# Performance work log

Measured on AMD Instinct MI355X. Metric: run time of the kernel, lower is better.

## Reference

```python
import jax, jax.numpy as jnp
import numpy as np

B, S, D, M = 4, 2048, 1024, 4  # batch, seq_len, d_model, n_stride_masks


def setup_inputs() -> dict:
    key = jax.random.key(0)
    ks = jax.random.split(key, 10)
    lin = lambda k: jax.random.normal(k, (D, D), jnp.float32) / np.float32(np.sqrt(D))
    return {
        "x": jax.random.normal(ks[0], (B, S, D), jnp.float32),
        "stride_masks": jax.random.randint(ks[1], (M, S, S), 0, 2, jnp.int32),
        "Wq": lin(ks[2]), "bq": jnp.zeros((D,), jnp.float32),
        "Wk": lin(ks[3]), "bk": jnp.zeros((D,), jnp.float32),
        "Wv": lin(ks[4]), "bv": jnp.zeros((D,), jnp.float32),
        "Wo": lin(ks[5]), "bo": jnp.zeros((D,), jnp.float32),
    }


def reference(x, stride_masks, Wq, bq, Wk, bk, Wv, bv, Wo, bo):
    scale = jnp.float32(np.sqrt(D))
    Q = x @ Wq + bq  # [B,S,D]
    K = x @ Wk + bk
    V = x @ Wv + bv
    # scores are identical for every mask; compute once (same math as the loop)
    scores = jnp.einsum("bqd,bkd->bqk", Q, K) / scale  # [B,S,S]
    masked = jnp.where(stride_masks[:, None] == 0, jnp.float32(-1e9), scores[None])  # [M,B,S,S]
    weights = jax.nn.softmax(masked, axis=-1)
    # sum over masks then divide by M == mean(stack(outs), 0)
    out = jnp.einsum("mbqk,bkd->bqd", weights, V) / jnp.float32(M)
    return out @ Wo + bo
```

## Files before the change

kernel.cpp:

```cpp
#include <hip/hip_runtime.h>
#include <hip/hip_bf16.h>
#include <stdint.h>

#define B_ 4
#define S_ 2048
#define D_ 1024
#define M_ 4

typedef __bf16 bf16;
typedef _Float16 f16;
typedef unsigned char u8;
typedef __bf16 bf16x8 __attribute__((ext_vector_type(8)));
typedef _Float16 f16x8 __attribute__((ext_vector_type(8)));
typedef float f32x4 __attribute__((ext_vector_type(4)));

__device__ __forceinline__ void async_copy16(const void* g, void* l) {
  __builtin_amdgcn_global_load_lds(
      (const __attribute__((address_space(1))) void*)g,
      (__attribute__((address_space(3))) void*)l, 16, 0, 0);
}

__global__ __launch_bounds__(256) void prep(
    const float* __restrict__ x, const float* __restrict__ w0,
    const float* __restrict__ w1, const float* __restrict__ w2,
    const float* __restrict__ w3, const int* __restrict__ masks,
    bf16* __restrict__ xc, bf16* __restrict__ WT, u8* __restrict__ pk) {
  __shared__ bf16 t[64][65];
  const int blk = blockIdx.x;
  const int tid = threadIdx.x;
  const long SS = (long)S_ * S_;

  if (blk < 4096) {
    const long i = (long)blk * 2048 + tid * 8;
    const float4 a = *(const float4*)(x + i);
    const float4 b = *(const float4*)(x + i + 4);
    bf16x8 o;
    o[0] = (bf16)a.x; o[1] = (bf16)a.y; o[2] = (bf16)a.z; o[3] = (bf16)a.w;
    o[4] = (bf16)b.x; o[5] = (bf16)b.y; o[6] = (bf16)b.z; o[7] = (bf16)b.w;
    *(bf16x8*)(xc + i) = o;
  } else if (blk < 5120) {
    const int local = blk - 4096;
    const int z = local >> 8;
    const int rem = local & 255;
    const int r0 = (rem >> 4) * 64;
    const int c0 = (rem & 15) * 64;
    const int tx = tid & 63;
    const int ty = tid >> 6;
    const float* in = (z == 0) ? w0 : (z == 1) ? w1 : (z == 2) ? w2 : w3;
    bf16* out = WT + (long)z * D_ * D_;
    for (int i = ty; i < 64; i += 4)
      t[i][tx] = (bf16)in[(long)(r0 + i) * D_ + c0 + tx];
    __syncthreads();
    for (int i = ty; i < 64; i += 4)
      out[(long)(c0 + i) * D_ + r0 + tx] = t[tx][i];
  } else {
    const long e = (long)(blk - 5120) * 2048 + tid * 8;
    unsigned long long wv = 0;
#pragma unroll
    for (int m = 0; m < M_; ++m) {
      const int4 a = *(const int4*)(masks + m * SS + e);
      const int4 b = *(const int4*)(masks + m * SS + e + 4);
      const int v[8] = {a.x, a.y, a.z, a.w, b.x, b.y, b.z, b.w};
#pragma unroll
      for (int j = 0; j < 8; ++j)
        wv |= (unsigned long long)(v[j] != 0 ? 1u : 0u) << (8 * j + m);
    }
    *(unsigned long long*)(pk + e) = wv;
  }
}

__global__ __launch_bounds__(256) void transposeB(
    const bf16* __restrict__ in, bf16* __restrict__ out,
    int rows, int cols, long ib, long ob) {
  __shared__ bf16 t[64][65];
  in += (long)blockIdx.z * ib;
  out += (long)blockIdx.z * ob;
  const int r0 = blockIdx.y * 64;
  const int c0 = blockIdx.x * 64;
  const int tx = threadIdx.x & 63;
  const int ty = threadIdx.x >> 6;
#pragma unroll
  for (int i = ty; i < 64; i += 4) t[i][tx] = in[(long)(r0 + i) * cols + c0 + tx];
  __syncthreads();
#pragma unroll
  for (int i = ty; i < 64; i += 4) out[(long)(c0 + i) * rows + r0 + tx] = t[tx][i];
}

#define MODE_PLAIN 0
#define MODE_EXP 1
#define MODE_QKV 2
#define MODE_PV 3

template <typename OutT, int MODE>
__global__ __launch_bounds__(512) void gemmA(
    const bf16* __restrict__ A, int lda,
    const bf16* __restrict__ Bt, long bzs, int ldb,
    OutT* __restrict__ C, int ldc,
    const float* __restrict__ bias0, const float* __restrict__ bias1,
    const float* __restrict__ bias2, float alpha, int K) {
  __shared__ __align__(16) bf16 As[3][256 * 32];
  __shared__ __align__(16) bf16 Bs[3][128 * 32];
  const int tid = threadIdx.x;
  const int lane = tid & 63;
  const int w = tid >> 6;
  const int wm = w & 3;
  const int wn = w >> 2;
  const int quad = lane >> 4;
  const int l15 = lane & 15;
  const int fse = (quad ^ ((l15 >> 1) & 3)) << 3;

  const int gx = gridDim.x;
  const int pid = blockIdx.y * gx + blockIdx.x;
  const int gsz = 8 * gx;
  const int bym = (pid / gsz) * 8 + (pid % 8);
  const int bxm = (pid % gsz) / 8;
  const int row0 = bym * 256;
  const int col0 = bxm * 128;

  const bf16* Arow = A + (long)row0 * lda;
  const bf16* Bcol;
  int grp = 0;
  if (MODE == MODE_QKV) {
    grp = col0 >> 10;
    Bcol = Bt + (long)grp * ((long)D_ * D_) + (long)(col0 & (D_ - 1)) * ldb;
  } else if (MODE == MODE_PV || MODE == MODE_EXP) {
    Bcol = Bt + (long)(row0 >> 11) * bzs + (long)col0 * ldb;
  } else {
    Bcol = Bt + (long)col0 * ldb;
  }

  const int sr = tid >> 2;
  const int sc = ((tid & 3) ^ ((tid >> 3) & 3)) << 3;
  const bf16* gA = Arow + (long)sr * lda + sc;
  const bf16* gB = Bcol + (long)sr * ldb + sc;
  const int dstoff = (tid >> 6) << 9;
  const long a128 = (long)128 * lda;

#define STAGE(h, s)                                                    \
  {                                                                    \
    const int kc_ = (h) * 32;                                          \
    bf16* da_ = &As[0][0] + (s) * (256 * 32) + dstoff;                 \
    bf16* db_ = &Bs[0][0] + (s) * (128 * 32) + dstoff;                 \
    async_copy16(gA + kc_, da_);                                       \
    async_copy16(gA + kc_ + a128, da_ + 4096);                         \
    async_copy16(gB + kc_, db_);                                       \
  }

#define READF(Ra, Rb, s)                                                   \
  {                                                                        \
    const bf16* pa_ = &As[0][0] + (s) * (256 * 32);                        \
    const bf16* pb_ = &Bs[0][0] + (s) * (128 * 32);                        \
    _Pragma("unroll") for (int j = 0; j < 4; ++j) {                        \
      Ra[j] = *(const bf16x8*)&pa_[(wm * 64 + j * 16 + l15) * 32 + fse];   \
      Rb[j] = *(const bf16x8*)&pb_[(wn * 64 + j * 16 + l15) * 32 + fse];   \
    }                                                                      \
  }

#define MM(Ra, Rb)                                                         \
  __builtin_amdgcn_s_setprio(1);                                           \
  _Pragma("unroll") for (int mi = 0; mi < 4; ++mi)                         \
      _Pragma("unroll") for (int ni = 0; ni < 4; ++ni) acc[mi][ni] =       \
          __builtin_amdgcn_mfma_f32_16x16x32_bf16(Ra[mi], Rb[ni],          \
                                                  acc[mi][ni], 0, 0, 0);   \
  __builtin_amdgcn_s_setprio(0);

  f32x4 acc[4][4];
#pragma unroll
  for (int i = 0; i < 4; ++i)
#pragma unroll
    for (int j = 0; j < 4; ++j) acc[i][j] = (f32x4){0.f, 0.f, 0.f, 0.f};

  const int nh = (K >> 6) << 1;

  STAGE(0, 0);
  STAGE(1, 1);
  asm volatile("s_waitcnt vmcnt(3)" ::: "memory");
  __builtin_amdgcn_s_barrier();
  __builtin_amdgcn_sched_barrier(0);

  int s0 = 0;
  for (int h = 0; h < nh; ++h) {
    bf16x8 af[4], bf[4];
    READF(af, bf, s0);
    if (h + 2 < nh) {
      const int s2 = (s0 >= 1) ? (s0 - 1) : 2;
      STAGE(h + 2, s2);
    }
    MM(af, bf);
    if (h + 2 < nh)
      asm volatile("s_waitcnt vmcnt(3)" ::: "memory");
    else if (h + 1 < nh)
      asm volatile("s_waitcnt vmcnt(0)" ::: "memory");
    if (h + 1 < nh) {
      __builtin_amdgcn_s_barrier();
      __builtin_amdgcn_sched_barrier(0);
    }
    s0 = (s0 == 2) ? 0 : (s0 + 1);
  }

#undef STAGE
#undef READF
#undef MM

  const float* bias = (MODE == MODE_QKV)
                          ? (grp == 0 ? bias0 : grp == 1 ? bias1 : bias2)
                          : bias0;
  const long NX = (long)B_ * S_ * D_;
  OutT* Cb = (MODE == MODE_QKV) ? C + (long)grp * NX : C;
#pragma unroll
  for (int mi = 0; mi < 4; ++mi)
#pragma unroll
    for (int ni = 0; ni < 4; ++ni) {
      const int col = col0 + wn * 64 + ni * 16 + l15;
      const int ccol = (MODE == MODE_QKV) ? (col & (D_ - 1)) : col;
      const float bv = bias ? bias[ccol] : 0.0f;
#pragma unroll
      for (int r = 0; r < 4; ++r) {
        const int row = row0 + wm * 64 + mi * 16 + quad * 4 + r;
        const float val = acc[mi][ni][r] * alpha + bv;
        if (MODE == MODE_EXP) {
          Cb[(long)row * ldc + col] = (OutT)__expf(val);
        } else if (MODE == MODE_QKV) {
          Cb[(long)row * D_ + ccol] = (OutT)val;
        } else {
          Cb[(long)row * ldc + col] = (OutT)val;
        }
      }
    }
}

__global__ __launch_bounds__(256) void softmax_combine(
    const f16* __restrict__ E, const u8* __restrict__ pk, bf16* __restrict__ P) {
  const int q = blockIdx.x;
  const int b = blockIdx.y;
  const int tid = threadIdx.x;
  const int lane = tid & 63;
  const int wv = tid >> 6;
  __shared__ float4 red[4];

  float e[8];
  {
    const f16x8 h = *(const f16x8*)(E + ((long)b * S_ + q) * S_ + tid * 8);
#pragma unroll
    for (int j = 0; j < 8; ++j) e[j] = (float)h[j];
  }
  const unsigned long long mb =
      *(const unsigned long long*)(pk + (long)q * S_ + tid * 8);

  float4 s = {0.f, 0.f, 0.f, 0.f};
#pragma unroll
  for (int j = 0; j < 8; ++j) {
    const unsigned bits = (unsigned)(mb >> (8 * j)) & 0xF;
    const float ev = e[j];
    if (bits & 1) s.x += ev;
    if (bits & 2) s.y += ev;
    if (bits & 4) s.z += ev;
    if (bits & 8) s.w += ev;
  }
#pragma unroll
  for (int o = 32; o > 0; o >>= 1) {
    s.x += __shfl_xor(s.x, o, 64);
    s.y += __shfl_xor(s.y, o, 64);
    s.z += __shfl_xor(s.z, o, 64);
    s.w += __shfl_xor(s.w, o, 64);
  }
  if (lane == 0) red[wv] = s;
  __syncthreads();
  const float4 t0 = red[0], t1 = red[1], t2 = red[2], t3 = red[3];
  const float r0 = 0.25f / (t0.x + t1.x + t2.x + t3.x);
  const float r1 = 0.25f / (t0.y + t1.y + t2.y + t3.y);
  const float r2 = 0.25f / (t0.z + t1.z + t2.z + t3.z);
  const float r3 = 0.25f / (t0.w + t1.w + t2.w + t3.w);

  bf16x8 o;
#pragma unroll
  for (int j = 0; j < 8; ++j) {
    const unsigned bits = (unsigned)(mb >> (8 * j)) & 0xF;
    const float wgt = ((bits & 1) ? r0 : 0.f) + ((bits & 2) ? r1 : 0.f) +
                      ((bits & 4) ? r2 : 0.f) + ((bits & 8) ? r3 : 0.f);
    o[j] = (bf16)(e[j] * wgt);
  }
  *(bf16x8*)(P + ((long)b * S_ + q) * S_ + tid * 8) = o;
}

extern "C" void kernel_launch(void* const* d_in, const int* in_sizes, int n_in,
                              void* d_out, int out_size, void* d_ws, size_t ws_size,
                              hipStream_t stream) {
  const float* x = (const float*)d_in[0];
  const int* masks = (const int*)d_in[1];
  const float* bq = (const float*)d_in[3];
  const float* bk = (const float*)d_in[5];
  const float* bv = (const float*)d_in[7];
  const float* bo = (const float*)d_in[9];
  float* out = (float*)d_out;

  const long DD = (long)D_ * D_;
  const long SD = (long)S_ * D_;
  const long NX = (long)B_ * SD;
  const long SS = (long)S_ * S_;

  bf16* xc = (bf16*)d_ws;
  bf16* WqT = xc + NX;
  bf16* WoT = WqT + 3 * DD;
  u8* pk = (u8*)(WoT + DD);
  bf16* Q = (bf16*)(pk + SS);
  bf16* K = Q + NX;
  bf16* V = K + NX;
  bf16* VT = V + NX;
  bf16* P = VT + NX;
  f16* E = (f16*)(P + (long)B_ * SS);
  bf16* attn = Q;

  dim3 blk(256);
  dim3 blk512(512);

  prep<<<dim3(7168), blk, 0, stream>>>(
      x, (const float*)d_in[2], (const float*)d_in[4], (const float*)d_in[6],
      (const float*)d_in[8], masks, xc, WqT, pk);

  gemmA<bf16, MODE_QKV><<<dim3(24, 32), blk512, 0, stream>>>(
      xc, D_, WqT, 0, D_, Q, D_, bq, bk, bv, 1.0f, D_);

  transposeB<<<dim3(16, 32, B_), blk, 0, stream>>>(V, VT, S_, D_, SD, SD);

  gemmA<f16, MODE_EXP><<<dim3(16, 32), blk512, 0, stream>>>(
      Q, D_, K, SD, D_, E, S_, nullptr, nullptr, nullptr, 1.0f / 32.0f, D_);

  softmax_combine<<<dim3(S_, B_), blk, 0, stream>>>(E, pk, P);

  gemmA<bf16, MODE_PV><<<dim3(8, 32), blk512, 0, stream>>>(
      P, S_, VT, SD, S_, attn, D_, nullptr, nullptr, nullptr, 1.0f, S_);

  gemmA<float, MODE_PLAIN><<<dim3(8, 32), blk512, 0, stream>>>(
      attn, D_, WoT, 0, D_, out, D_, bo, nullptr, nullptr, 1.0f, D_);
}
```

Baseline: 348.4 us.

## Add 256-thread 256x128-tile GEMM with triple-buffered LDS for QKV and scores

Introduces a new GEMM kernel (gemmB) using 256 threads with each wave computing a 128x64 sub-tile, so every wave holds 8x4 MFMA accumulators. It uses a three-stage async global-to-LDS pipeline with 32-wide K steps and MFMA priority raising. The QKV projection and exp-score GEMMs switch to it from the 512-thread gemmA. This raises per-wave data reuse and register use and changes the pipeline depth, at the cost of lower occupancy and more register pressure.

```diff
diff --git a/kernel.cpp b/kernel.cpp
--- a/kernel.cpp
+++ b/kernel.cpp
@@ -229,6 +229,148 @@
     }
 }
 
+template <typename OutT, int MODE>
+__global__ __launch_bounds__(256) void gemmB(
+    const bf16* __restrict__ A, int lda,
+    const bf16* __restrict__ Bt, long bzs, int ldb,
+    OutT* __restrict__ C, int ldc,
+    const float* __restrict__ bias0, const float* __restrict__ bias1,
+    const float* __restrict__ bias2, float alpha, int K) {
+  __shared__ __align__(16) bf16 As[3][256 * 32];
+  __shared__ __align__(16) bf16 Bs[3][128 * 32];
+  const int tid = threadIdx.x;
+  const int lane = tid & 63;
+  const int w = tid >> 6;
+  const int wm = w & 1;
+  const int wn = w >> 1;
+  const int quad = lane >> 4;
+  const int l15 = lane & 15;
+  const int fse = (quad ^ ((l15 >> 1) & 3)) << 3;
+
+  const int gx = gridDim.x;
+  const int pid = blockIdx.y * gx + blockIdx.x;
+  const int gsz = 8 * gx;
+  const int bym = (pid / gsz) * 8 + (pid % 8);
+  const int bxm = (pid % gsz) / 8;
+  const int row0 = bym * 256;
+  const int col0 = bxm * 128;
+
+  const bf16* Arow = A + (long)row0 * lda;
+  const bf16* Bcol;
+  int grp = 0;
+  if (MODE == MODE_QKV) {
+    grp = col0 >> 10;
+    Bcol = Bt + (long)grp * ((long)D_ * D_) + (long)(col0 & (D_ - 1)) * ldb;
+  } else if (MODE == MODE_PV || MODE == MODE_EXP) {
+    Bcol = Bt + (long)(row0 >> 11) * bzs + (long)col0 * ldb;
+  } else {
+    Bcol = Bt + (long)col0 * ldb;
+  }
+
+  const int sr = tid >> 2;
+  const int sc = ((tid & 3) ^ ((tid >> 3) & 3)) << 3;
+  const bf16* gA = Arow + (long)sr * lda + sc;
+  const bf16* gB = Bcol + (long)sr * ldb + sc;
+  const int dstoff = (tid >> 6) << 9;
+  const long a64 = (long)64 * lda;
+  const long b64 = (long)64 * ldb;
+
+#define STAGE(h, s)                                                    \
+  {                                                                    \
+    const int kc_ = (h) * 32;                                          \
+    bf16* da_ = &As[0][0] + (s) * (256 * 32) + dstoff;                 \
+    bf16* db_ = &Bs[0][0] + (s) * (128 * 32) + dstoff;                 \
+    async_copy16(gA + kc_, da_);                                       \
+    async_copy16(gA + kc_ + a64, da_ + 2048);                          \
+    async_copy16(gA + kc_ + 2 * a64, da_ + 4096);                      \
+    async_copy16(gA + kc_ + 3 * a64, da_ + 6144);                      \
+    async_copy16(gB + kc_, db_);                                       \
+    async_copy16(gB + kc_ + b64, db_ + 2048);                          \
+  }
+
+#define READF(Ra, Rb, s)                                                    \
+  {                                                                         \
+    const bf16* pa_ = &As[0][0] + (s) * (256 * 32);                         \
+    const bf16* pb_ = &Bs[0][0] + (s) * (128 * 32);                         \
+    _Pragma("unroll") for (int j = 0; j < 8; ++j)                           \
+        Ra[j] = *(const bf16x8*)&pa_[(wm * 128 + j * 16 + l15) * 32 + fse]; \
+    _Pragma("unroll") for (int j = 0; j < 4; ++j)                           \
+        Rb[j] = *(const bf16x8*)&pb_[(wn * 64 + j * 16 + l15) * 32 + fse];  \
+  }
+
+#define MM(Ra, Rb)                                                         \
+  __builtin_amdgcn_s_setprio(1);                                           \
+  _Pragma("unroll") for (int mi = 0; mi < 8; ++mi)                         \
+      _Pragma("unroll") for (int ni = 0; ni < 4; ++ni) acc[mi][ni] =       \
+          __builtin_amdgcn_mfma_f32_16x16x32_bf16(Ra[mi], Rb[ni],          \
+                                                  acc[mi][ni], 0, 0, 0);   \
+  __builtin_amdgcn_s_setprio(0);
+
+  f32x4 acc[8][4];
+#pragma unroll
+  for (int i = 0; i < 8; ++i)
+#pragma unroll
+    for (int j = 0; j < 4; ++j) acc[i][j] = (f32x4){0.f, 0.f, 0.f, 0.f};
+
+  const int nh = (K >> 6) << 1;
+
+  STAGE(0, 0);
+  STAGE(1, 1);
+  asm volatile("s_waitcnt vmcnt(6)" ::: "memory");
+  __builtin_amdgcn_s_barrier();
+  __builtin_amdgcn_sched_barrier(0);
+
+  int s0 = 0;
+  for (int h = 0; h < nh; ++h) {
+    bf16x8 af[8], bf[4];
+    READF(af, bf, s0);
+    if (h + 2 < nh) {
+      const int s2 = (s0 >= 1) ? (s0 - 1) : 2;
+      STAGE(h + 2, s2);
+    }
+    MM(af, bf);
+    if (h + 2 < nh)
+      asm volatile("s_waitcnt vmcnt(6)" ::: "memory");
+    else if (h + 1 < nh)
+      asm volatile("s_waitcnt vmcnt(0)" ::: "memory");
+    if (h + 1 < nh) {
+      __builtin_amdgcn_s_barrier();
+      __builtin_amdgcn_sched_barrier(0);
+    }
+    s0 = (s0 == 2) ? 0 : (s0 + 1);
+  }
+
+#undef STAGE
+#undef READF
+#undef MM
+
+  const float* bias = (MODE == MODE_QKV)
+                          ? (grp == 0 ? bias0 : grp == 1 ? bias1 : bias2)
+                          : bias0;
+  const long NX = (long)B_ * S_ * D_;
+  OutT* Cb = (MODE == MODE_QKV) ? C + (long)grp * NX : C;
+#pragma unroll
+  for (int mi = 0; mi < 8; ++mi)
+#pragma unroll
+    for (int ni = 0; ni < 4; ++ni) {
+      const int col = col0 + wn * 64 + ni * 16 + l15;
+      const int ccol = (MODE == MODE_QKV) ? (col & (D_ - 1)) : col;
+      const float bv = bias ? bias[ccol] : 0.0f;
+#pragma unroll
+      for (int r = 0; r < 4; ++r) {
+        const int row = row0 + wm * 128 + mi * 16 + quad * 4 + r;
+        const float val = acc[mi][ni][r] * alpha + bv;
+        if (MODE == MODE_EXP) {
+          Cb[(long)row * ldc + col] = (OutT)__expf(val);
+        } else if (MODE == MODE_QKV) {
+          Cb[(long)row * D_ + ccol] = (OutT)val;
+        } else {
+          Cb[(long)row * ldc + col] = (OutT)val;
+        }
+      }
+    }
+}
+
 __global__ __launch_bounds__(256) void softmax_combine(
     const f16* __restrict__ E, const u8* __restrict__ pk, bf16* __restrict__ P) {
   const int q = blockIdx.x;
@@ -318,12 +460,12 @@
       x, (const float*)d_in[2], (const float*)d_in[4], (const float*)d_in[6],
       (const float*)d_in[8], masks, xc, WqT, pk);
 
-  gemmA<bf16, MODE_QKV><<<dim3(24, 32), blk512, 0, stream>>>(
+  gemmB<bf16, MODE_QKV><<<dim3(24, 32), blk, 0, stream>>>(
       xc, D_, WqT, 0, D_, Q, D_, bq, bk, bv, 1.0f, D_);
 
   transposeB<<<dim3(16, 32, B_), blk, 0, stream>>>(V, VT, S_, D_, SD, SD);
 
-  gemmA<f16, MODE_EXP><<<dim3(16, 32), blk512, 0, stream>>>(
+  gemmB<f16, MODE_EXP><<<dim3(16, 32), blk, 0, stream>>>(
       Q, D_, K, SD, D_, E, S_, nullptr, nullptr, nullptr, 1.0f / 32.0f, D_);
 
   softmax_combine<<<dim3(S_, B_), blk, 0, stream>>>(E, pk, P);
```

Result: slower. 393.4 us (+12.9%).
